# Optimization experiments

Measured on AMD Instinct MI355X. Metric: run time of the kernel, lower is better.

## Reference

```python
import jax, jax.numpy as jnp
import numpy as np

N_NODES = 50000
N_EDGES = 800000
D = 128
BN_EPS = 1e-5


def gcn_conv(x, src, dst, W, b, n_nodes):
    # x: [N, Din]; src/dst: [E+N] (self-loops already appended)
    h = x @ W  # [N, Dout]
    deg = jax.ops.segment_sum(jnp.ones_like(src, dtype=h.dtype), dst, num_segments=n_nodes)
    dinv = jnp.where(deg > 0, jax.lax.rsqrt(deg), 0.0)  # deg^{-1/2}
    norm = dinv[src] * dinv[dst]  # [E+N]
    msg = h[src] * norm[:, None]  # gather + scale
    out = jax.ops.segment_sum(msg, dst, num_segments=n_nodes)  # scatter-add
    return out + b


def batchnorm_prelu(x, gamma, beta, a):
    # training-mode BN over node dim (biased variance), then PReLU
    mu = jnp.mean(x, axis=0)
    var = jnp.mean(jnp.square(x - mu), axis=0)
    xn = (x - mu) * jax.lax.rsqrt(var + BN_EPS)
    y = xn * gamma + beta
    return jnp.where(y >= 0, y, a * y)


def setup_inputs():
    key = jax.random.key(0)
    ks = jax.random.split(key, 8)
    x = jax.random.normal(ks[0], (N_NODES, D), dtype=jnp.float32)
    edge_index = jax.random.randint(ks[1], (2, N_EDGES), 0, N_NODES, dtype=jnp.int32)
    lim = float(np.sqrt(6.0 / (D + D)))  # glorot
    W1 = jax.random.uniform(ks[2], (D, D), jnp.float32, -lim, lim)
    W2 = jax.random.uniform(ks[3], (D, D), jnp.float32, -lim, lim)
    b1 = jnp.zeros((D,), jnp.float32)
    b2 = jnp.zeros((D,), jnp.float32)
    gamma1 = jnp.ones((D,), jnp.float32)
    beta1 = jnp.zeros((D,), jnp.float32)
    gamma2 = jnp.ones((D,), jnp.float32)
    beta2 = jnp.zeros((D,), jnp.float32)
    a1 = jnp.full((1,), 0.25, jnp.float32)
    a2 = jnp.full((1,), 0.25, jnp.float32)
    return {"x": x, "edge_index": edge_index, "W1": W1, "b1": b1, "gamma1": gamma1,
            "beta1": beta1, "a1": a1, "W2": W2, "b2": b2, "gamma2": gamma2,
            "beta2": beta2, "a2": a2}


def reference(x, edge_index, W1, b1, gamma1, beta1, a1, W2, b2, gamma2, beta2, a2):
    n = x.shape[0]
    loops = jnp.arange(n, dtype=edge_index.dtype)
    src = jnp.concatenate([edge_index[0], loops])
    dst = jnp.concatenate([edge_index[1], loops])
    h = gcn_conv(x, src, dst, W1, b1, n)
    h = batchnorm_prelu(h, gamma1, beta1, a1)
    h = gcn_conv(h, src, dst, W2, b2, n)
    h = batchnorm_prelu(h, gamma2, beta2, a2)
    return h
```

## Files before the change

### kernel.cpp

```cpp
#include <hip/hip_runtime.h>
#include <hip/hip_bf16.h>

#define N_NODES 50000
#define N_EDGES 800000
#define D 128
#define BN_EPS 1e-5f
#define SCAN_BLOCKS ((N_NODES + 255) / 256)
#define GEMM_ROWS 128
#define LDS_PITCH 136

typedef unsigned short u16;
typedef short bf16x8 __attribute__((ext_vector_type(8)));
typedef float f32x4  __attribute__((ext_vector_type(4)));

__device__ __forceinline__ u16 f2bf(float f) {
    union { float f; unsigned int u; } v; v.f = f;
    unsigned int u = v.u;
    return (u16)((u + 0x7FFF + ((u >> 16) & 1)) >> 16);
}
__device__ __forceinline__ float bflo(unsigned int u) {
    union { unsigned int u; float f; } v; v.u = u << 16; return v.f;
}
__device__ __forceinline__ float bfhi(unsigned int u) {
    union { unsigned int u; float f; } v; v.u = u & 0xFFFF0000u; return v.f;
}
__device__ __forceinline__ unsigned int packbf(float a, float b) {
    return (unsigned int)f2bf(a) | ((unsigned int)f2bf(b) << 16);
}

__global__ void deg_count(const int* __restrict__ dst, int* __restrict__ cnt) {
    int e = blockIdx.x * blockDim.x + threadIdx.x;
    if (e < N_EDGES) atomicAdd(&cnt[dst[e]], 1);
}

__global__ __launch_bounds__(256) void scan_local(const int* __restrict__ cnt,
                                                  int* __restrict__ row_ptr,
                                                  int* __restrict__ partials,
                                                  float* __restrict__ dinv) {
    __shared__ int s[256];
    const int t = threadIdx.x;
    const int i = blockIdx.x * 256 + t;
    int v = (i < N_NODES) ? cnt[i] : 0;
    if (i < N_NODES) dinv[i] = rsqrtf((float)v + 1.0f);
    s[t] = v;
    __syncthreads();
#pragma unroll
    for (int off = 1; off < 256; off <<= 1) {
        int add = (t >= off) ? s[t - off] : 0;
        __syncthreads();
        s[t] += add;
        __syncthreads();
    }
    if (i < N_NODES) row_ptr[i] = s[t] - v;
    if (t == 255) partials[blockIdx.x] = s[255];
}

__global__ __launch_bounds__(256) void scan_partials(int* __restrict__ partials) {
    __shared__ int s[256];
    const int t = threadIdx.x;
    int v = (t < SCAN_BLOCKS) ? partials[t] : 0;
    s[t] = v;
    __syncthreads();
#pragma unroll
    for (int off = 1; off < 256; off <<= 1) {
        int add = (t >= off) ? s[t - off] : 0;
        __syncthreads();
        s[t] += add;
        __syncthreads();
    }
    if (t < SCAN_BLOCKS) partials[t] = s[t] - v;
}

__global__ __launch_bounds__(256) void scan_apply(int* __restrict__ row_ptr,
                                                  const int* __restrict__ partials,
                                                  int* __restrict__ cursor) {
    const int i = blockIdx.x * 256 + threadIdx.x;
    if (i < N_NODES) {
        int r = row_ptr[i] + partials[blockIdx.x];
        row_ptr[i] = r;
        cursor[i]  = r;
    }
    if (i == 0) row_ptr[N_NODES] = N_EDGES;
}

__global__ void csr_fill(const int* __restrict__ src, const int* __restrict__ dst,
                         int* __restrict__ cursor, int* __restrict__ col) {
    int e = blockIdx.x * blockDim.x + threadIdx.x;
    if (e < N_EDGES) {
        int d = dst[e];
        int p = atomicAdd(&cursor[d], 1);
        col[p] = src[e];
    }
}

__global__ __launch_bounds__(256) void w_prep(const float* __restrict__ W1,
                                              const float* __restrict__ W2,
                                              u16* __restrict__ Wt1,
                                              u16* __restrict__ Wt2) {
    int t = blockIdx.x * blockDim.x + threadIdx.x;
    const float* W = (t < 16384) ? W1 : W2;
    u16* Wt        = (t < 16384) ? Wt1 : Wt2;
    int u = t & 16383;
    int k = u >> 7, n = u & 127;
    Wt[n * 128 + k] = f2bf(W[u]);
}

template <bool BN_IN>
__global__ __launch_bounds__(256) void gemm_bf16(const void* __restrict__ Xv,
                                                 const u16* __restrict__ Wt,
                                                 u16* __restrict__ C,
                                                 const float* __restrict__ dinv,
                                                 const float* __restrict__ sums,
                                                 const float* __restrict__ gamma,
                                                 const float* __restrict__ beta,
                                                 const float* __restrict__ a,
                                                 int nrows) {
    __shared__ u16 As[GEMM_ROWS * LDS_PITCH];
    __shared__ u16 Ws[128 * LDS_PITCH];
    const int tid  = threadIdx.x;
    const int row0 = blockIdx.x * GEMM_ROWS;
    const float invN = 1.0f / (float)N_NODES;

    const bf16x8* Wt8 = (const bf16x8*)Wt;
#pragma unroll
    for (int i = 0; i < 8; ++i) {
        int u = tid + 256 * i;
        int n = u >> 4, kg = u & 15;
        *(bf16x8*)&Ws[n * LDS_PITCH + kg * 8] = Wt8[u];
    }

    if (BN_IN) {
        const uint4* X4 = (const uint4*)Xv;
        const float av = a[0];
#pragma unroll
        for (int i = 0; i < 8; ++i) {
            int u    = tid + 256 * i;
            int r    = u >> 4, kg = u & 15;
            int grow = row0 + r;
            uint4 o = make_uint4(0, 0, 0, 0);
            if (grow < nrows) {
                uint4 v = X4[(size_t)grow * 16 + kg];
                float f[8] = { bflo(v.x), bfhi(v.x), bflo(v.y), bfhi(v.y),
                               bflo(v.z), bfhi(v.z), bflo(v.w), bfhi(v.w) };
#pragma unroll
                for (int c = 0; c < 8; ++c) {
                    int fe     = kg * 8 + c;
                    float mean = sums[fe] * invN;
                    float var  = sums[128 + fe] * invN - mean * mean;
                    float sc   = rsqrtf(var + BN_EPS) * gamma[fe];
                    float y    = (f[c] - mean) * sc + beta[fe];
                    f[c]       = (y >= 0.f) ? y : av * y;
                }
                o.x = packbf(f[0], f[1]); o.y = packbf(f[2], f[3]);
                o.z = packbf(f[4], f[5]); o.w = packbf(f[6], f[7]);
            }
            *(uint4*)&As[r * LDS_PITCH + kg * 8] = o;
        }
    } else {
        const float4* X4 = (const float4*)Xv;
#pragma unroll
        for (int i = 0; i < 16; ++i) {
            int u    = tid + 256 * i;
            int r    = u >> 5, kf = u & 31;
            int grow = row0 + r;
            float4 v = make_float4(0.f, 0.f, 0.f, 0.f);
            if (grow < nrows) v = X4[(size_t)grow * 32 + kf];
            ushort4 p;
            p.x = f2bf(v.x); p.y = f2bf(v.y); p.z = f2bf(v.z); p.w = f2bf(v.w);
            *(ushort4*)&As[r * LDS_PITCH + kf * 4] = p;
        }
    }
    __syncthreads();

    const int wv   = tid >> 6;
    const int lane = tid & 63;
    const int n    = lane & 15;
    const int q    = lane >> 4;
    const int c0   = wv * 32;

    bf16x8 bfr[4][2];
#pragma unroll
    for (int kb = 0; kb < 4; ++kb)
#pragma unroll
        for (int c = 0; c < 2; ++c)
            bfr[kb][c] = *(const bf16x8*)&Ws[(c0 + 16 * c + n) * LDS_PITCH + 32 * kb + 8 * q];

    f32x4 acc[8][2];
    const f32x4 z = {0.f, 0.f, 0.f, 0.f};
#pragma unroll
    for (int rt = 0; rt < 8; ++rt) { acc[rt][0] = z; acc[rt][1] = z; }

#pragma unroll
    for (int kb = 0; kb < 4; ++kb) {
#pragma unroll
        for (int rt = 0; rt < 8; ++rt) {
            bf16x8 af = *(const bf16x8*)&As[(16 * rt + n) * LDS_PITCH + 32 * kb + 8 * q];
            acc[rt][0] = __builtin_amdgcn_mfma_f32_16x16x32_bf16(af, bfr[kb][0], acc[rt][0], 0, 0, 0);
            acc[rt][1] = __builtin_amdgcn_mfma_f32_16x16x32_bf16(af, bfr[kb][1], acc[rt][1], 0, 0, 0);
        }
    }

#pragma unroll
    for (int rt = 0; rt < 8; ++rt) {
        int gr0 = row0 + 16 * rt + 4 * q;
#pragma unroll
        for (int r = 0; r < 4; ++r) {
            int gr = gr0 + r;
            if (gr < nrows) {
                float dv = dinv[gr];
                C[(size_t)gr * D + c0 + n]      = f2bf(acc[rt][0][r] * dv);
                C[(size_t)gr * D + c0 + 16 + n] = f2bf(acc[rt][1][r] * dv);
            }
        }
    }
}

__global__ __launch_bounds__(256) void pull_agg(const u16* __restrict__ H,
                                                const int* __restrict__ row_ptr,
                                                const int* __restrict__ col,
                                                const float* __restrict__ dinv,
                                                u16* __restrict__ out) {
    const int sub  = threadIdx.x & 15;
    const int grp  = (blockIdx.x * blockDim.x + threadIdx.x) >> 4;
    const int ngrp = (gridDim.x * blockDim.x) >> 4;
    const uint4* H4   = (const uint4*)H;
    uint4*       out4 = (uint4*)out;

    for (int d = grp; d < N_NODES; d += ngrp) {
        const int beg = row_ptr[d];
        const int end = row_ptr[d + 1];
        float a0[8], a1[8] = {}, a2[8] = {}, a3[8] = {};
        {
            uint4 v = H4[(size_t)d * 16 + sub];
            a0[0] = bflo(v.x); a0[1] = bfhi(v.x); a0[2] = bflo(v.y); a0[3] = bfhi(v.y);
            a0[4] = bflo(v.z); a0[5] = bfhi(v.z); a0[6] = bflo(v.w); a0[7] = bfhi(v.w);
        }
        int j = beg;
        for (; j + 3 < end; j += 4) {
            const int s0 = col[j], s1 = col[j + 1], s2 = col[j + 2], s3 = col[j + 3];
            const uint4 v0 = H4[(size_t)s0 * 16 + sub];
            const uint4 v1 = H4[(size_t)s1 * 16 + sub];
            const uint4 v2 = H4[(size_t)s2 * 16 + sub];
            const uint4 v3 = H4[(size_t)s3 * 16 + sub];
            a0[0] += bflo(v0.x); a0[1] += bfhi(v0.x); a0[2] += bflo(v0.y); a0[3] += bfhi(v0.y);
            a0[4] += bflo(v0.z); a0[5] += bfhi(v0.z); a0[6] += bflo(v0.w); a0[7] += bfhi(v0.w);
            a1[0] += bflo(v1.x); a1[1] += bfhi(v1.x); a1[2] += bflo(v1.y); a1[3] += bfhi(v1.y);
            a1[4] += bflo(v1.z); a1[5] += bfhi(v1.z); a1[6] += bflo(v1.w); a1[7] += bfhi(v1.w);
            a2[0] += bflo(v2.x); a2[1] += bfhi(v2.x); a2[2] += bflo(v2.y); a2[3] += bfhi(v2.y);
            a2[4] += bflo(v2.z); a2[5] += bfhi(v2.z); a2[6] += bflo(v2.w); a2[7] += bfhi(v2.w);
            a3[0] += bflo(v3.x); a3[1] += bfhi(v3.x); a3[2] += bflo(v3.y); a3[3] += bfhi(v3.y);
            a3[4] += bflo(v3.z); a3[5] += bfhi(v3.z); a3[6] += bflo(v3.w); a3[7] += bfhi(v3.w);
        }
        for (; j < end; ++j) {
            const uint4 v = H4[(size_t)col[j] * 16 + sub];
            a0[0] += bflo(v.x); a0[1] += bfhi(v.x); a0[2] += bflo(v.y); a0[3] += bfhi(v.y);
            a0[4] += bflo(v.z); a0[5] += bfhi(v.z); a0[6] += bflo(v.w); a0[7] += bfhi(v.w);
        }
        const float dv = dinv[d];
        float r[8];
#pragma unroll
        for (int c = 0; c < 8; ++c) r[c] = ((a0[c] + a1[c]) + (a2[c] + a3[c])) * dv;
        uint4 o;
        o.x = packbf(r[0], r[1]); o.y = packbf(r[2], r[3]);
        o.z = packbf(r[4], r[5]); o.w = packbf(r[6], r[7]);
        out4[(size_t)d * 16 + sub] = o;
    }
}

__global__ __launch_bounds__(256) void bn_reduce_bf(const u16* __restrict__ X,
                                                    float* __restrict__ sums, int n) {
    __shared__ float red[256];
    const int fp  = threadIdx.x & 63;
    const int rof = threadIdx.x >> 6;
    const unsigned int* X2 = (const unsigned int*)X;
    float s0 = 0.f, q0 = 0.f, s1 = 0.f, q1 = 0.f;
    for (int r = blockIdx.x * 4 + rof; r < n; r += gridDim.x * 4) {
        unsigned int u = X2[(size_t)r * 64 + fp];
        float v0 = bflo(u), v1 = bfhi(u);
        s0 += v0; q0 += v0 * v0; s1 += v1; q1 += v1 * v1;
    }
    red[threadIdx.x] = s0; __syncthreads();
    if (rof == 0) s0 = red[fp] + red[fp + 64] + red[fp + 128] + red[fp + 192];
    __syncthreads(); red[threadIdx.x] = q0; __syncthreads();
    if (rof == 0) q0 = red[fp] + red[fp + 64] + red[fp + 128] + red[fp + 192];
    __syncthreads(); red[threadIdx.x] = s1; __syncthreads();
    if (rof == 0) s1 = red[fp] + red[fp + 64] + red[fp + 128] + red[fp + 192];
    __syncthreads(); red[threadIdx.x] = q1; __syncthreads();
    if (rof == 0) {
        q1 = red[fp] + red[fp + 64] + red[fp + 128] + red[fp + 192];
        int f = fp * 2;
        atomicAdd(&sums[f], s0);       atomicAdd(&sums[128 + f], q0);
        atomicAdd(&sums[f + 1], s1);   atomicAdd(&sums[128 + f + 1], q1);
    }
}

__global__ void bn_prelu_bf(const u16* __restrict__ X, const float* __restrict__ sums,
                            const float* __restrict__ gamma, const float* __restrict__ beta,
                            const float* __restrict__ a, float* __restrict__ out,
                            float invN) {
    int idx = blockIdx.x * blockDim.x + threadIdx.x;
    if (idx >= N_NODES * 64) return;
    unsigned int u = ((const unsigned int*)X)[idx];
    int f0 = (idx * 2) & 127;
    float av = a[0];
    float2 o;
    {
        float mean = sums[f0] * invN;
        float var  = sums[128 + f0] * invN - mean * mean;
        float sc   = rsqrtf(var + BN_EPS) * gamma[f0];
        float y    = (bflo(u) - mean) * sc + beta[f0];
        o.x = (y >= 0.f) ? y : av * y;
    }
    {
        int f1 = f0 + 1;
        float mean = sums[f1] * invN;
        float var  = sums[128 + f1] * invN - mean * mean;
        float sc   = rsqrtf(var + BN_EPS) * gamma[f1];
        float y    = (bfhi(u) - mean) * sc + beta[f1];
        o.y = (y >= 0.f) ? y : av * y;
    }
    ((float2*)out)[idx] = o;
}

extern "C" void kernel_launch(void* const* d_in, const int* in_sizes, int n_in,
                              void* d_out, int out_size, void* d_ws, size_t ws_size,
                              hipStream_t stream) {
    const float* x      = (const float*)d_in[0];
    const int*   edges  = (const int*)d_in[1];
    const float* W1     = (const float*)d_in[2];
    const float* gamma1 = (const float*)d_in[4];
    const float* beta1  = (const float*)d_in[5];
    const float* a1     = (const float*)d_in[6];
    const float* W2     = (const float*)d_in[7];
    const float* gamma2 = (const float*)d_in[9];
    const float* beta2  = (const float*)d_in[10];
    const float* a2     = (const float*)d_in[11];

    const int* src = edges;
    const int* dst = edges + N_EDGES;

    float* OUT = (float*)d_out;
    char* ws = (char*)d_ws;
    u16*   Abf      = (u16*)ws;    ws += (size_t)N_NODES * D * sizeof(u16);
    u16*   Obf      = (u16*)ws;    ws += (size_t)N_NODES * D * sizeof(u16);
    float* dinv     = (float*)ws;  ws += N_NODES * sizeof(float);
    float* sums     = (float*)ws;  ws += 256 * sizeof(float);
    int*   cnt      = (int*)ws;    ws += N_NODES * sizeof(int);
    int*   cursor   = (int*)ws;    ws += N_NODES * sizeof(int);
    int*   row_ptr  = (int*)ws;    ws += (N_NODES + 1) * sizeof(int);
    int*   partials = (int*)ws;    ws += 256 * sizeof(int);
    u16*   Wt1      = (u16*)ws;    ws += 16384 * sizeof(u16);
    u16*   Wt2      = (u16*)ws;    ws += 16384 * sizeof(u16);
    int*   col      = (int*)ws;    ws += (size_t)N_EDGES * sizeof(int);

    const float invN = 1.0f / (float)N_NODES;

    const int eGrid    = (N_EDGES + 255) / 256;
    const int gemmGrid = (N_NODES + GEMM_ROWS - 1) / GEMM_ROWS;
    const int prGrid   = (N_NODES * 64 + 255) / 256;

    hipMemsetAsync(cnt, 0, N_NODES * sizeof(int), stream);
    deg_count<<<eGrid, 256, 0, stream>>>(dst, cnt);
    scan_local<<<SCAN_BLOCKS, 256, 0, stream>>>(cnt, row_ptr, partials, dinv);
    scan_partials<<<1, 256, 0, stream>>>(partials);
    scan_apply<<<SCAN_BLOCKS, 256, 0, stream>>>(row_ptr, partials, cursor);
    csr_fill<<<eGrid, 256, 0, stream>>>(src, dst, cursor, col);
    w_prep<<<128, 256, 0, stream>>>(W1, W2, Wt1, Wt2);

    gemm_bf16<false><<<gemmGrid, 256, 0, stream>>>(x, Wt1, Abf, dinv,
                                                   nullptr, nullptr, nullptr, nullptr, N_NODES);
    pull_agg<<<2048, 256, 0, stream>>>(Abf, row_ptr, col, dinv, Obf);
    hipMemsetAsync(sums, 0, 256 * sizeof(float), stream);
    bn_reduce_bf<<<512, 256, 0, stream>>>(Obf, sums, N_NODES);

    gemm_bf16<true><<<gemmGrid, 256, 0, stream>>>(Obf, Wt2, Abf, dinv,
                                                  sums, gamma1, beta1, a1, N_NODES);
    pull_agg<<<2048, 256, 0, stream>>>(Abf, row_ptr, col, dinv, Obf);
    hipMemsetAsync(sums, 0, 256 * sizeof(float), stream);
    bn_reduce_bf<<<512, 256, 0, stream>>>(Obf, sums, N_NODES);
    bn_prelu_bf<<<prGrid, 256, 0, stream>>>(Obf, sums, gamma2, beta2, a2, OUT, invN);
}
```

Before: 370.4 us.

## Build CSR via two-level bucket sort in LDS with 16-bit column indices

Replaces the global-atomic degree count, three-kernel scan and atomic CSR fill with a bucketed radix-style build. Edges are first histogrammed and scattered into 196 destination buckets of 256 nodes each, using per-tile LDS sorting, and each bucket is then sorted into CSR order in LDS. That also produces row_ptr and dinv. Column indices are stored as u16, which halves the index traffic in the aggregation kernels. In exchange it assumes node ids fit in 16 bits and that no bucket exceeds REC_CAP edges, so a skewed degree distribution would silently drop edges.

New measurement: 310.1 us. 16.3% less time.

```diff
diff --git a/kernel.cpp b/kernel.cpp
--- a/kernel.cpp
+++ b/kernel.cpp
@@ -5,9 +5,14 @@
 #define N_EDGES 800000
 #define D 128
 #define BN_EPS 1e-5f
-#define SCAN_BLOCKS ((N_NODES + 255) / 256)
 #define GEMM_ROWS 128
 #define LDS_PITCH 136
+
+#define BSH 8
+#define NB 196
+#define TILE 4096
+#define NTILES ((N_EDGES + TILE - 1) / TILE)
+#define REC_CAP 6144
 
 typedef unsigned short u16;
 typedef short bf16x8 __attribute__((ext_vector_type(8)));
@@ -28,20 +33,29 @@
     return (unsigned int)f2bf(a) | ((unsigned int)f2bf(b) << 16);
 }
 
-__global__ void deg_count(const int* __restrict__ dst, int* __restrict__ cnt) {
-    int e = blockIdx.x * blockDim.x + threadIdx.x;
-    if (e < N_EDGES) atomicAdd(&cnt[dst[e]], 1);
-}
-
-__global__ __launch_bounds__(256) void scan_local(const int* __restrict__ cnt,
-                                                  int* __restrict__ row_ptr,
-                                                  int* __restrict__ partials,
-                                                  float* __restrict__ dinv) {
+__global__ __launch_bounds__(256) void bucket_hist(const int* __restrict__ dst,
+                                                   int* __restrict__ btot) {
+    __shared__ int h[256];
+    const int t  = threadIdx.x;
+    const int e0 = blockIdx.x * TILE;
+    h[t] = 0;
+    __syncthreads();
+#pragma unroll
+    for (int i = 0; i < 16; ++i) {
+        int e = e0 + t + 256 * i;
+        if (e < N_EDGES) atomicAdd(&h[dst[e] >> BSH], 1);
+    }
+    __syncthreads();
+    if (t < NB && h[t] > 0) atomicAdd(&btot[t], h[t]);
+}
+
+__global__ __launch_bounds__(256) void bucket_scan(const int* __restrict__ btot,
+                                                   int* __restrict__ bbase,
+                                                   int* __restrict__ bcur,
+                                                   int* __restrict__ row_ptr) {
     __shared__ int s[256];
     const int t = threadIdx.x;
-    const int i = blockIdx.x * 256 + t;
-    int v = (i < N_NODES) ? cnt[i] : 0;
-    if (i < N_NODES) dinv[i] = rsqrtf((float)v + 1.0f);
+    int v = (t < NB) ? btot[t] : 0;
     s[t] = v;
     __syncthreads();
 #pragma unroll
@@ -51,46 +65,118 @@
         s[t] += add;
         __syncthreads();
     }
-    if (i < N_NODES) row_ptr[i] = s[t] - v;
-    if (t == 255) partials[blockIdx.x] = s[255];
-}
-
-__global__ __launch_bounds__(256) void scan_partials(int* __restrict__ partials) {
-    __shared__ int s[256];
-    const int t = threadIdx.x;
-    int v = (t < SCAN_BLOCKS) ? partials[t] : 0;
-    s[t] = v;
+    if (t < NB) { bbase[t] = s[t] - v; bcur[t] = s[t] - v; }
+    if (t == 0) row_ptr[N_NODES] = N_EDGES;
+}
+
+__global__ __launch_bounds__(256) void bucket_scatter(const int* __restrict__ src,
+                                                      const int* __restrict__ dst,
+                                                      int* __restrict__ bcur,
+                                                      unsigned int* __restrict__ brec) {
+    __shared__ int h[256];
+    __shared__ int sb[256];
+    __shared__ int lbase[256];
+    __shared__ int lcur[256];
+    __shared__ int gbase[256];
+    __shared__ unsigned int  rec[TILE];
+    __shared__ unsigned char rbk[TILE];
+    const int t  = threadIdx.x;
+    const int e0 = blockIdx.x * TILE;
+    const int tcount = min(TILE, N_EDGES - e0);
+
+    h[t] = 0;
+    __syncthreads();
+
+    unsigned int myrec[16];
+    int          myb[16];
+#pragma unroll
+    for (int i = 0; i < 16; ++i) {
+        int e = e0 + t + 256 * i;
+        if (e < N_EDGES) {
+            unsigned int s_ = (unsigned int)src[e];
+            unsigned int d_ = (unsigned int)dst[e];
+            int b = (int)(d_ >> BSH);
+            myb[i]   = b;
+            myrec[i] = s_ | ((d_ & 255u) << 16);
+            atomicAdd(&h[b], 1);
+        } else myb[i] = -1;
+    }
+    __syncthreads();
+    sb[t] = h[t];
     __syncthreads();
 #pragma unroll
     for (int off = 1; off < 256; off <<= 1) {
-        int add = (t >= off) ? s[t - off] : 0;
-        __syncthreads();
-        s[t] += add;
-        __syncthreads();
-    }
-    if (t < SCAN_BLOCKS) partials[t] = s[t] - v;
-}
-
-__global__ __launch_bounds__(256) void scan_apply(int* __restrict__ row_ptr,
-                                                  const int* __restrict__ partials,
-                                                  int* __restrict__ cursor) {
-    const int i = blockIdx.x * 256 + threadIdx.x;
-    if (i < N_NODES) {
-        int r = row_ptr[i] + partials[blockIdx.x];
-        row_ptr[i] = r;
-        cursor[i]  = r;
-    }
-    if (i == 0) row_ptr[N_NODES] = N_EDGES;
-}
-
-__global__ void csr_fill(const int* __restrict__ src, const int* __restrict__ dst,
-                         int* __restrict__ cursor, int* __restrict__ col) {
-    int e = blockIdx.x * blockDim.x + threadIdx.x;
-    if (e < N_EDGES) {
-        int d = dst[e];
-        int p = atomicAdd(&cursor[d], 1);
-        col[p] = src[e];
-    }
+        int add = (t >= off) ? sb[t - off] : 0;
+        __syncthreads();
+        sb[t] += add;
+        __syncthreads();
+    }
+    lbase[t] = sb[t] - h[t];
+    lcur[t]  = sb[t] - h[t];
+    __syncthreads();
+#pragma unroll
+    for (int i = 0; i < 16; ++i) {
+        if (myb[i] >= 0) {
+            int p = atomicAdd(&lcur[myb[i]], 1);
+            rec[p] = myrec[i];
+            rbk[p] = (unsigned char)myb[i];
+        }
+    }
+    __syncthreads();
+    if (t < NB && h[t] > 0) gbase[t] = atomicAdd(&bcur[t], h[t]);
+    __syncthreads();
+    for (int i = t; i < tcount; i += 256) {
+        int b = rbk[i];
+        brec[gbase[b] + (i - lbase[b])] = rec[i];
+    }
+}
+
+__global__ __launch_bounds__(256) void bucket_csr(const unsigned int* __restrict__ brec,
+                                                  const int* __restrict__ bbase,
+                                                  const int* __restrict__ btot,
+                                                  int* __restrict__ row_ptr,
+                                                  u16* __restrict__ col,
+                                                  float* __restrict__ dinv) {
+    __shared__ unsigned int rec[REC_CAP];
+    __shared__ u16 cls[REC_CAP];
+    __shared__ int h[256];
+    __shared__ int sb[256];
+    __shared__ int lcur[256];
+    const int b    = blockIdx.x;
+    const int t    = threadIdx.x;
+    const int base = bbase[b];
+    const int cnt  = min(btot[b], REC_CAP);
+    const int n0   = b << BSH;
+    const int nn   = min(256, N_NODES - n0);
+
+    for (int i = t; i < cnt; i += 256) rec[i] = brec[base + i];
+    h[t] = 0;
+    __syncthreads();
+    for (int i = t; i < cnt; i += 256) atomicAdd(&h[(rec[i] >> 16) & 255u], 1);
+    __syncthreads();
+    sb[t] = h[t];
+    __syncthreads();
+#pragma unroll
+    for (int off = 1; off < 256; off <<= 1) {
+        int add = (t >= off) ? sb[t - off] : 0;
+        __syncthreads();
+        sb[t] += add;
+        __syncthreads();
+    }
+    int excl = sb[t] - h[t];
+    lcur[t] = excl;
+    if (t < nn) {
+        row_ptr[n0 + t] = base + excl;
+        dinv[n0 + t]    = rsqrtf((float)h[t] + 1.0f);
+    }
+    __syncthreads();
+    for (int i = t; i < cnt; i += 256) {
+        unsigned int r = rec[i];
+        int p = atomicAdd(&lcur[(r >> 16) & 255u], 1);
+        cls[p] = (u16)(r & 0xFFFFu);
+    }
+    __syncthreads();
+    for (int i = t; i < cnt; i += 256) col[base + i] = cls[i];
 }
 
 __global__ __launch_bounds__(256) void w_prep(const float* __restrict__ W1,
@@ -217,7 +303,7 @@
 
 __global__ __launch_bounds__(256) void pull_agg(const u16* __restrict__ H,
                                                 const int* __restrict__ row_ptr,
-                                                const int* __restrict__ col,
+                                                const u16* __restrict__ col,
                                                 const float* __restrict__ dinv,
                                                 u16* __restrict__ out) {
     const int sub  = threadIdx.x & 15;
@@ -345,26 +431,24 @@
     u16*   Obf      = (u16*)ws;    ws += (size_t)N_NODES * D * sizeof(u16);
     float* dinv     = (float*)ws;  ws += N_NODES * sizeof(float);
     float* sums     = (float*)ws;  ws += 256 * sizeof(float);
-    int*   cnt      = (int*)ws;    ws += N_NODES * sizeof(int);
-    int*   cursor   = (int*)ws;    ws += N_NODES * sizeof(int);
     int*   row_ptr  = (int*)ws;    ws += (N_NODES + 1) * sizeof(int);
-    int*   partials = (int*)ws;    ws += 256 * sizeof(int);
+    int*   btot     = (int*)ws;    ws += NB * sizeof(int);
+    int*   bbase    = (int*)ws;    ws += NB * sizeof(int);
+    int*   bcur     = (int*)ws;    ws += NB * sizeof(int);
+    unsigned int* brec = (unsigned int*)ws; ws += (size_t)N_EDGES * sizeof(unsigned int);
+    u16*   col      = (u16*)ws;    ws += (size_t)N_EDGES * sizeof(u16);
     u16*   Wt1      = (u16*)ws;    ws += 16384 * sizeof(u16);
     u16*   Wt2      = (u16*)ws;    ws += 16384 * sizeof(u16);
-    int*   col      = (int*)ws;    ws += (size_t)N_EDGES * sizeof(int);
 
     const float invN = 1.0f / (float)N_NODES;
-
-    const int eGrid    = (N_EDGES + 255) / 256;
     const int gemmGrid = (N_NODES + GEMM_ROWS - 1) / GEMM_ROWS;
     const int prGrid   = (N_NODES * 64 + 255) / 256;
 
-    hipMemsetAsync(cnt, 0, N_NODES * sizeof(int), stream);
-    deg_count<<<eGrid, 256, 0, stream>>>(dst, cnt);
-    scan_local<<<SCAN_BLOCKS, 256, 0, stream>>>(cnt, row_ptr, partials, dinv);
-    scan_partials<<<1, 256, 0, stream>>>(partials);
-    scan_apply<<<SCAN_BLOCKS, 256, 0, stream>>>(row_ptr, partials, cursor);
-    csr_fill<<<eGrid, 256, 0, stream>>>(src, dst, cursor, col);
+    hipMemsetAsync(btot, 0, NB * sizeof(int), stream);
+    bucket_hist<<<NTILES, 256, 0, stream>>>(dst, btot);
+    bucket_scan<<<1, 256, 0, stream>>>(btot, bbase, bcur, row_ptr);
+    bucket_scatter<<<NTILES, 256, 0, stream>>>(src, dst, bcur, brec);
+    bucket_csr<<<NB, 256, 0, stream>>>(brec, bbase, btot, row_ptr, col, dinv);
     w_prep<<<128, 256, 0, stream>>>(W1, W2, Wt1, Wt2);
 
     gemm_bf16<false><<<gemmGrid, 256, 0, stream>>>(x, Wt1, Abf, dinv,
```
